# Kernel optimization log

Hardware: AMD Instinct MI355X
Metric: run time of the kernel (lower is better)

Reference implementation:

```python
import jax, jax.numpy as jnp
import numpy as np

N_A = 50000
N_B = 50000
E = 500000
D = 128


def setup_inputs() -> dict:
    key = jax.random.key(0)
    ks = jax.random.split(key, 16)
    s = 0.02
    inp = {
        "x_a": jax.random.normal(ks[0], (N_A, D), jnp.float32),
        "x_b": jax.random.normal(ks[1], (N_B, D), jnp.float32),
        # shared GraphEdgeWeight params
        "Wp": jax.random.normal(ks[2], (D, D), jnp.float32) * s,
        "bp": jnp.zeros((D,), jnp.float32),
        "Wc": jax.random.normal(ks[3], (D, D), jnp.float32) * s,
        "bc": jnp.zeros((D,), jnp.float32),
        "W1": jax.random.normal(ks[4], (D, 3 * D), jnp.float32) * s,
        "b1": jnp.zeros((D,), jnp.float32),
        "W2": jax.random.normal(ks[5], (1, D), jnp.float32) * s,
        "b2": jnp.zeros((1,), jnp.float32),
        # GraphConv params for edge type A->B
        "Wrel_ab": jax.random.normal(ks[6], (D, D), jnp.float32) * s,
        "brel_ab": jnp.zeros((D,), jnp.float32),
        "Wroot_ab": jax.random.normal(ks[7], (D, D), jnp.float32) * s,
        "broot_ab": jnp.zeros((D,), jnp.float32),
        # GraphConv params for edge type B->A
        "Wrel_ba": jax.random.normal(ks[8], (D, D), jnp.float32) * s,
        "brel_ba": jnp.zeros((D,), jnp.float32),
        "Wroot_ba": jax.random.normal(ks[9], (D, D), jnp.float32) * s,
        "broot_ba": jnp.zeros((D,), jnp.float32),
        # edge indices: row0 = src node ids, row1 = dst node ids
        "ei_ab": jax.random.randint(ks[10], (2, E), 0, N_A),
        "ei_ba": jax.random.randint(ks[11], (2, E), 0, N_B),
    }
    return inp


def _edge_type_conv(x_src, x_dst, ei, Wp, bp, Wc, bc, W1, b1, W2, b2,
                    Wrel, brel, Wroot, broot, n_dst):
    # gather endpoint features per edge  [E, D]
    par = x_src[ei[0]]
    cld = x_dst[ei[1]]
    # GraphEdgeWeight: encoders (Linear + LeakyReLU; dropout inactive in eval)
    ep = jax.nn.leaky_relu(par @ Wp.T + bp, negative_slope=0.01)
    ec = jax.nn.leaky_relu(cld @ Wc.T + bc, negative_slope=0.01)
    feat = jnp.concatenate([ep, ec, jnp.abs(par - cld)], axis=-1)  # [E, 3D]
    h = jax.nn.relu(feat @ W1.T + b1)                              # [E, D]
    w = jax.nn.sigmoid(h @ W2.T + b2)[:, 0]                        # [E]
    # GraphConv: out_i = Wrel @ sum_{j->i} w_e x_j + Wroot @ x_i (+ biases)
    msg = jax.ops.segment_sum(par * w[:, None], ei[1], num_segments=n_dst)
    return msg @ Wrel.T + brel + x_dst @ Wroot.T + broot


def reference(x_a, x_b, Wp, bp, Wc, bc, W1, b1, W2, b2,
              Wrel_ab, brel_ab, Wroot_ab, broot_ab,
              Wrel_ba, brel_ba, Wroot_ba, broot_ba,
              ei_ab, ei_ba):
    out_b = _edge_type_conv(x_a, x_b, ei_ab, Wp, bp, Wc, bc, W1, b1, W2, b2,
                            Wrel_ab, brel_ab, Wroot_ab, broot_ab, N_B)
    out_a = _edge_type_conv(x_b, x_a, ei_ba, Wp, bp, Wc, bc, W1, b1, W2, b2,
                            Wrel_ba, brel_ba, Wroot_ba, broot_ba, N_A)
    return out_a, out_b
```

## Files before the change

kernel.cpp:

```cpp
#include <hip/hip_runtime.h>
#include <hip/hip_bf16.h>

typedef unsigned short u16;
typedef __attribute__((ext_vector_type(8))) short bf16x8;
typedef __attribute__((ext_vector_type(2))) short s16x2;
typedef __attribute__((ext_vector_type(4))) float f32x4;

#define N_NODES 50000
#define EDGES 500000
#define WPT 31250
#define NWAVES 3125
#define NBLK 782

__device__ __forceinline__ u16 f2bf(float f) {
  return __builtin_bit_cast(u16, __float2bfloat16(f));
}
__device__ __forceinline__ float bf2f(u16 u) {
  return __builtin_bit_cast(float, ((unsigned)u) << 16);
}
__device__ __forceinline__ float bfe(bf16x8 v, int j) {
  return bf2f((u16)v[j]);
}

__device__ __forceinline__ void pk_atomic_bf16(u16* addr, float lo, float hi) {
#if __has_builtin(__builtin_amdgcn_global_atomic_fadd_v2bf16)
  s16x2 v;
  v[0] = (short)f2bf(lo);
  v[1] = (short)f2bf(hi);
  __builtin_amdgcn_global_atomic_fadd_v2bf16(
      (__attribute__((address_space(1))) s16x2*)addr, v);
#else
  unsigned* p = (unsigned*)addr;
  unsigned old = *p, assumed;
  do {
    assumed = old;
    float l2 = bf2f((u16)(assumed & 0xffff)) + lo;
    float h2 = bf2f((u16)(assumed >> 16)) + hi;
    unsigned nv = (unsigned)f2bf(l2) | ((unsigned)f2bf(h2) << 16);
    old = atomicCAS(p, assumed, nv);
  } while (old != assumed);
#endif
}

__global__ __launch_bounds__(256) void prep_weights(
    const float* __restrict__ Wp, const float* __restrict__ Wc,
    const float* __restrict__ W1,
    const float* __restrict__ Wrel_ab, const float* __restrict__ Wroot_ab,
    const float* __restrict__ Wrel_ba, const float* __restrict__ Wroot_ba,
    u16* __restrict__ out)
{
  int tid = blockIdx.x * 256 + threadIdx.x;
  int m = tid >> 14;
  int idx = tid & 16383;
  int r = idx >> 7;
  int c = idx & 127;
  float val;
  switch (m) {
    case 0: val = Wp[r * 128 + c]; break;
    case 1: val = Wc[r * 128 + c]; break;
    case 2: val = W1[r * 384 + c]; break;
    case 3: val = W1[r * 384 + 128 + c]; break;
    case 4: val = W1[r * 384 + 256 + c]; break;
    case 5: val = Wrel_ab[r * 128 + c]; break;
    case 6: val = Wroot_ab[r * 128 + c]; break;
    case 7: val = Wrel_ba[r * 128 + c]; break;
    default: val = Wroot_ba[r * 128 + c]; break;
  }
  out[tid] = f2bf(val);
}

__global__ __launch_bounds__(256) void cast_x(
    const float* __restrict__ xa, const float* __restrict__ xb,
    u16* __restrict__ oa, u16* __restrict__ ob)
{
  int t = blockIdx.x * 256 + threadIdx.x;
  const int HALF = (N_NODES * 128) / 8;
  const float* src;
  u16* dst;
  int idx;
  if (t < HALF) { src = xa; dst = oa; idx = t * 8; }
  else          { src = xb; dst = ob; idx = (t - HALF) * 8; }
  f32x4 a = *(const f32x4*)(src + idx);
  f32x4 b = *(const f32x4*)(src + idx + 4);
  bf16x8 o;
#pragma unroll
  for (int j = 0; j < 4; j++) {
    o[j]     = (short)f2bf(a[j]);
    o[j + 4] = (short)f2bf(b[j]);
  }
  *(bf16x8*)(dst + idx) = o;
}

__global__ __launch_bounds__(256) void encoder2(
    const u16* __restrict__ xa_bf, const u16* __restrict__ xb_bf,
    const u16* __restrict__ Wp_b, const float* __restrict__ bp,
    const u16* __restrict__ Wc_b, const float* __restrict__ bc,
    const u16* __restrict__ W1a_b, const float* __restrict__ b1,
    const u16* __restrict__ W1b_b,
    u16* __restrict__ u_a, u16* __restrict__ v_a,
    u16* __restrict__ u_b, u16* __restrict__ v_b)
{
  __shared__ u16 tile[4][2176];
  int widx = threadIdx.x >> 6;
  int w = blockIdx.x * 4 + widx;
  int type = (w >= NBLK * 4) ? 1 : 0;
  int nw = w - type * NBLK * 4;
  if (nw >= NWAVES) nw = NWAVES - 1;
  const u16* xbf = type ? xb_bf : xa_bf;
  u16* u_out = type ? u_b : u_a;
  u16* v_out = type ? v_b : v_a;
  int row0 = nw * 16;
  int lane = threadIdx.x & 63;
  int col = lane & 15;
  int quad = lane >> 4;
  u16* tl = tile[widx];

  bf16x8 af[4];
#pragma unroll
  for (int ks = 0; ks < 4; ks++)
    af[ks] = *(const bf16x8*)(xbf + (size_t)(row0 + col) * 128 + ks * 32 + quad * 8);

  f32x4 zero = {0.f, 0.f, 0.f, 0.f};

  for (int chain = 0; chain < 2; chain++) {
    const u16* Wenc = chain ? Wc_b : Wp_b;
    const float* benc = chain ? bc : bp;
    const u16* Wmix = chain ? W1b_b : W1a_b;
    const float* bmix = chain ? nullptr : b1;
    u16* outp = chain ? v_out : u_out;

    f32x4 acc[8];
#pragma unroll
    for (int nt = 0; nt < 8; nt++) acc[nt] = zero;
#pragma unroll
    for (int ks = 0; ks < 4; ks++) {
      const u16* wp = Wenc + col * 128 + ks * 32 + quad * 8;
#pragma unroll
      for (int nt = 0; nt < 8; nt++) {
        bf16x8 bf = *(const bf16x8*)(wp + nt * 2048);
        acc[nt] = __builtin_amdgcn_mfma_f32_16x16x32_bf16(af[ks], bf, acc[nt], 0, 0, 0);
      }
    }
    __syncthreads();
#pragma unroll
    for (int nt = 0; nt < 8; nt++) {
      float be = benc[nt * 16 + col];
#pragma unroll
      for (int r = 0; r < 4; r++) {
        float v = acc[nt][r] + be;
        v = v > 0.f ? v : 0.01f * v;
        tl[(quad * 4 + r) * 136 + nt * 16 + col] = f2bf(v);
      }
    }
    __syncthreads();
    bf16x8 a2[4];
#pragma unroll
    for (int ks = 0; ks < 4; ks++)
      a2[ks] = *(const bf16x8*)&tl[col * 136 + ks * 32 + quad * 8];

    f32x4 acc2[8];
#pragma unroll
    for (int nt = 0; nt < 8; nt++) acc2[nt] = zero;
#pragma unroll
    for (int ks = 0; ks < 4; ks++) {
      const u16* wp = Wmix + col * 128 + ks * 32 + quad * 8;
#pragma unroll
      for (int nt = 0; nt < 8; nt++) {
        bf16x8 bf = *(const bf16x8*)(wp + nt * 2048);
        acc2[nt] = __builtin_amdgcn_mfma_f32_16x16x32_bf16(a2[ks], bf, acc2[nt], 0, 0, 0);
      }
    }
#pragma unroll
    for (int nt = 0; nt < 8; nt++) {
      float bm = bmix ? bmix[nt * 16 + col] : 0.f;
#pragma unroll
      for (int r = 0; r < 4; r++)
        outp[(size_t)(row0 + quad * 4 + r) * 128 + nt * 16 + col] = f2bf(acc2[nt][r] + bm);
    }
  }
}

__global__ __launch_bounds__(256) void y_gemm2(
    const u16* __restrict__ xa_bf, const u16* __restrict__ xb_bf,
    const u16* __restrict__ Wrelab_b, const u16* __restrict__ Wrelba_b,
    u16* __restrict__ y_ab, u16* __restrict__ y_ba)
{
  int w = blockIdx.x * 4 + (threadIdx.x >> 6);
  int type = (w >= NBLK * 4) ? 1 : 0;
  int nw = w - type * NBLK * 4;
  if (nw >= NWAVES) return;
  const u16* xbf = type ? xb_bf : xa_bf;
  const u16* Wb = type ? Wrelba_b : Wrelab_b;
  u16* yout = type ? y_ba : y_ab;
  int row0 = nw * 16;
  int lane = threadIdx.x & 63;
  int col = lane & 15;
  int quad = lane >> 4;

  bf16x8 af[4];
#pragma unroll
  for (int ks = 0; ks < 4; ks++)
    af[ks] = *(const bf16x8*)(xbf + (size_t)(row0 + col) * 128 + ks * 32 + quad * 8);

  f32x4 zero = {0.f, 0.f, 0.f, 0.f};
  f32x4 acc[8];
#pragma unroll
  for (int nt = 0; nt < 8; nt++) acc[nt] = zero;
#pragma unroll
  for (int ks = 0; ks < 4; ks++) {
    const u16* wp = Wb + col * 128 + ks * 32 + quad * 8;
#pragma unroll
    for (int nt = 0; nt < 8; nt++) {
      bf16x8 bf = *(const bf16x8*)(wp + nt * 2048);
      acc[nt] = __builtin_amdgcn_mfma_f32_16x16x32_bf16(af[ks], bf, acc[nt], 0, 0, 0);
    }
  }
#pragma unroll
  for (int nt = 0; nt < 8; nt++)
#pragma unroll
    for (int r = 0; r < 4; r++)
      yout[(size_t)(row0 + quad * 4 + r) * 128 + nt * 16 + col] = f2bf(acc[nt][r]);
}

__global__ __launch_bounds__(256) void out_gemm2(
    const u16* __restrict__ xa_bf, const u16* __restrict__ xb_bf,
    const u16* __restrict__ msgY_a, const u16* __restrict__ msgY_b,
    const u16* __restrict__ Wrootba_b, const u16* __restrict__ Wrootab_b,
    const float* __restrict__ brel_ba, const float* __restrict__ broot_ba,
    const float* __restrict__ brel_ab, const float* __restrict__ broot_ab,
    float* __restrict__ out_a, float* __restrict__ out_b)
{
  int w = blockIdx.x * 4 + (threadIdx.x >> 6);
  int type = (w >= NBLK * 4) ? 1 : 0;
  int nw = w - type * NBLK * 4;
  if (nw >= NWAVES) return;
  const u16* xbf = type ? xb_bf : xa_bf;
  const u16* msgY = type ? msgY_b : msgY_a;
  const u16* Wb = type ? Wrootab_b : Wrootba_b;
  const float* brel = type ? brel_ab : brel_ba;
  const float* broot = type ? broot_ab : broot_ba;
  float* outp = type ? out_b : out_a;
  int row0 = nw * 16;
  int lane = threadIdx.x & 63;
  int col = lane & 15;
  int quad = lane >> 4;

  bf16x8 af[4];
#pragma unroll
  for (int ks = 0; ks < 4; ks++)
    af[ks] = *(const bf16x8*)(xbf + (size_t)(row0 + col) * 128 + ks * 32 + quad * 8);

  f32x4 zero = {0.f, 0.f, 0.f, 0.f};
  f32x4 acc[8];
#pragma unroll
  for (int nt = 0; nt < 8; nt++) acc[nt] = zero;
#pragma unroll
  for (int ks = 0; ks < 4; ks++) {
    const u16* wp = Wb + col * 128 + ks * 32 + quad * 8;
#pragma unroll
    for (int nt = 0; nt < 8; nt++) {
      bf16x8 bf = *(const bf16x8*)(wp + nt * 2048);
      acc[nt] = __builtin_amdgcn_mfma_f32_16x16x32_bf16(af[ks], bf, acc[nt], 0, 0, 0);
    }
  }
#pragma unroll
  for (int nt = 0; nt < 8; nt++) {
    int c = nt * 16 + col;
    float b = brel[c] + broot[c];
#pragma unroll
    for (int r = 0; r < 4; r++) {
      size_t row = row0 + quad * 4 + r;
      outp[row * 128 + c] = acc[nt][r] + b + bf2f(msgY[row * 128 + c]);
    }
  }
}

__global__ __launch_bounds__(256) void edge_fused(
    const u16* __restrict__ xa_bf, const u16* __restrict__ xb_bf,
    const int* __restrict__ ei_ab, const int* __restrict__ ei_ba,
    const u16* __restrict__ W1c,
    const u16* __restrict__ u_a, const u16* __restrict__ v_a,
    const u16* __restrict__ u_b, const u16* __restrict__ v_b,
    const u16* __restrict__ y_ab, const u16* __restrict__ y_ba,
    const float* __restrict__ W2, const float* __restrict__ b2p,
    u16* __restrict__ msgY_a, u16* __restrict__ msgY_b)
{
  __shared__ u16 tld[4][2176];
  int widx = threadIdx.x >> 6;
  int w = blockIdx.x * 4 + widx;
  int type = (w >= WPT) ? 1 : 0;
  int e0 = (w - type * WPT) * 16;
  const u16* xs = type ? xb_bf : xa_bf;
  const u16* xd = type ? xa_bf : xb_bf;
  const int* ei = type ? ei_ba : ei_ab;
  const u16* uT = type ? u_b : u_a;
  const u16* vT = type ? v_a : v_b;
  const u16* yT = type ? y_ba : y_ab;
  u16* msgY     = type ? msgY_a : msgY_b;

  int lane = threadIdx.x & 63;
  int col = lane & 15;
  int quad = lane >> 4;

  int em = e0 + col;
  int si = ei[em];
  int di = ei[EDGES + em];

  bf16x8 af[4];
#pragma unroll
  for (int ks = 0; ks < 4; ks++) {
    bf16x8 s8 = *(const bf16x8*)(xs + (size_t)si * 128 + ks * 32 + quad * 8);
    bf16x8 d8 = *(const bf16x8*)(xd + (size_t)di * 128 + ks * 32 + quad * 8);
#pragma unroll
    for (int j = 0; j < 8; j++)
      af[ks][j] = (short)f2bf(__builtin_fabsf(bfe(s8, j) - bfe(d8, j)));
  }

  f32x4 zero = {0.f, 0.f, 0.f, 0.f};
  f32x4 acc[8];
#pragma unroll
  for (int nt = 0; nt < 8; nt++) acc[nt] = zero;
#pragma unroll
  for (int ks = 0; ks < 4; ks++) {
    const u16* wp = W1c + col * 128 + ks * 32 + quad * 8;
#pragma unroll
    for (int nt = 0; nt < 8; nt++) {
      bf16x8 bf = *(const bf16x8*)(wp + nt * 2048);
      acc[nt] = __builtin_amdgcn_mfma_f32_16x16x32_bf16(af[ks], bf, acc[nt], 0, 0, 0);
    }
  }

  u16* tl = tld[widx];
#pragma unroll
  for (int nt = 0; nt < 8; nt++)
#pragma unroll
    for (int r = 0; r < 4; r++)
      tl[(quad * 4 + r) * 136 + nt * 16 + col] = f2bf(acc[nt][r]);
  __syncthreads();

  int e = e0 + (lane >> 2);
  int s2 = ei[e];
  int d2 = ei[EDGES + e];
  int c0 = (lane & 3) * 32;
  const u16* trow = &tl[(lane >> 2) * 136 + c0];
  const u16* urow = uT + (size_t)s2 * 128 + c0;
  const u16* vrow = vT + (size_t)d2 * 128 + c0;

  float p = 0.f;
#pragma unroll
  for (int k = 0; k < 4; k++) {
    bf16x8 tt = *(const bf16x8*)(trow + k * 8);
    bf16x8 uu = *(const bf16x8*)(urow + k * 8);
    bf16x8 vv = *(const bf16x8*)(vrow + k * 8);
    f32x4 w0 = *(const f32x4*)(W2 + c0 + k * 8);
    f32x4 w1 = *(const f32x4*)(W2 + c0 + k * 8 + 4);
#pragma unroll
    for (int j = 0; j < 4; j++) {
      float q0 = bfe(tt, j) + bfe(uu, j) + bfe(vv, j);
      if (q0 > 0.f) p += q0 * w0[j];
      float q1 = bfe(tt, j + 4) + bfe(uu, j + 4) + bfe(vv, j + 4);
      if (q1 > 0.f) p += q1 * w1[j];
    }
  }
  p += __shfl_xor(p, 1, 64);
  p += __shfl_xor(p, 2, 64);
  float wgt = 1.f / (1.f + __expf(-(p + b2p[0])));

#pragma unroll
  for (int r = 0; r < 4; r++) {
    int src_lane = (quad * 4 + r) * 4;
    float wr = __shfl(wgt, src_lane, 64);
    int sr = __shfl(s2, src_lane, 64);
    int dr = __shfl(d2, src_lane, 64);
    const u16* yrow = yT + (size_t)sr * 128;
    u16* mrow = msgY + (size_t)dr * 128;
#pragma unroll
    for (int nt = 0; nt < 4; nt++) {
      int c = nt * 32 + col * 2;
      unsigned yv = *(const unsigned*)(yrow + c);
      pk_atomic_bf16(mrow + c, wr * bf2f((u16)(yv & 0xffff)),
                               wr * bf2f((u16)(yv >> 16)));
    }
  }
}

extern "C" void kernel_launch(void* const* d_in, const int* in_sizes, int n_in,
                              void* d_out, int out_size, void* d_ws, size_t ws_size,
                              hipStream_t stream) {
  const float* x_a      = (const float*)d_in[0];
  const float* x_b      = (const float*)d_in[1];
  const float* Wp       = (const float*)d_in[2];
  const float* bp       = (const float*)d_in[3];
  const float* Wc       = (const float*)d_in[4];
  const float* bc       = (const float*)d_in[5];
  const float* W1       = (const float*)d_in[6];
  const float* b1       = (const float*)d_in[7];
  const float* W2       = (const float*)d_in[8];
  const float* b2       = (const float*)d_in[9];
  const float* Wrel_ab  = (const float*)d_in[10];
  const float* brel_ab  = (const float*)d_in[11];
  const float* Wroot_ab = (const float*)d_in[12];
  const float* broot_ab = (const float*)d_in[13];
  const float* Wrel_ba  = (const float*)d_in[14];
  const float* brel_ba  = (const float*)d_in[15];
  const float* Wroot_ba = (const float*)d_in[16];
  const float* broot_ba = (const float*)d_in[17];
  const int*   ei_ab    = (const int*)d_in[18];
  const int*   ei_ba    = (const int*)d_in[19];

  char* ws = (char*)d_ws;
  u16* Wb        = (u16*)ws;
  u16* Wp_b      = Wb + 0 * 16384;
  u16* Wc_b      = Wb + 1 * 16384;
  u16* W1a_b     = Wb + 2 * 16384;
  u16* W1b_b     = Wb + 3 * 16384;
  u16* W1c_b     = Wb + 4 * 16384;
  u16* Wrelab_b  = Wb + 5 * 16384;
  u16* Wrootab_b = Wb + 6 * 16384;
  u16* Wrelba_b  = Wb + 7 * 16384;
  u16* Wrootba_b = Wb + 8 * 16384;

  u16* xa_bf   = (u16*)(ws + 1048576);
  u16* xb_bf   = (u16*)(ws + 13848576);
  u16* u_a     = (u16*)(ws + 26648576);
  u16* v_a     = (u16*)(ws + 39448576);
  u16* u_b     = (u16*)(ws + 52248576);
  u16* v_b     = (u16*)(ws + 65048576);
  u16* y_ab    = (u16*)(ws + 77848576);
  u16* y_ba    = (u16*)(ws + 90648576);
  u16* msgY_a  = (u16*)(ws + 103448576);
  u16* msgY_b  = (u16*)(ws + 116248576);

  float* out_a = (float*)d_out;
  float* out_b = out_a + (size_t)N_NODES * 128;

  hipMemsetAsync(msgY_a, 0, (size_t)2 * N_NODES * 128 * sizeof(u16), stream);

  prep_weights<<<576, 256, 0, stream>>>(Wp, Wc, W1, Wrel_ab, Wroot_ab,
                                        Wrel_ba, Wroot_ba, Wb);
  cast_x<<<6250, 256, 0, stream>>>(x_a, x_b, xa_bf, xb_bf);

  encoder2<<<2 * NBLK, 256, 0, stream>>>(xa_bf, xb_bf, Wp_b, bp, Wc_b, bc,
                                         W1a_b, b1, W1b_b, u_a, v_a, u_b, v_b);
  y_gemm2<<<2 * NBLK, 256, 0, stream>>>(xa_bf, xb_bf, Wrelab_b, Wrelba_b, y_ab, y_ba);

  edge_fused<<<15625, 256, 0, stream>>>(xa_bf, xb_bf, ei_ab, ei_ba, W1c_b,
                                        u_a, v_a, u_b, v_b, y_ab, y_ba,
                                        W2, b2, msgY_a, msgY_b);

  out_gemm2<<<2 * NBLK, 256, 0, stream>>>(xa_bf, xb_bf, msgY_a, msgY_b,
                                          Wrootba_b, Wrootab_b,
                                          brel_ba, broot_ba, brel_ab, broot_ab,
                                          out_a, out_b);
}
```

Baseline: 772.2 us.

## Aggregate raw source features instead of pre-projected Y and fold Wrel into output GEMM

Drops the y_gemm2 pre-projection kernel. The edge kernel now scatters weighted raw source features, taken from the already-gathered xs rows held in LDS, instead of gathering a separate projected row per edge. The output GEMM then applies Wrel to the aggregated message alongside Wroot in one MFMA loop. This removes a kernel launch and a random gather of 25.6MB of y data per edge, and adds one extra GEMM over the nodes. It also removes several __syncthreads in the encoder and edge kernels, which risks LDS races because the tl buffers are per-wave.

```diff
diff --git a/kernel.cpp b/kernel.cpp
--- a/kernel.cpp
+++ b/kernel.cpp
@@ -141,7 +141,6 @@
         acc[nt] = __builtin_amdgcn_mfma_f32_16x16x32_bf16(af[ks], bf, acc[nt], 0, 0, 0);
       }
     }
-    __syncthreads();
 #pragma unroll
     for (int nt = 0; nt < 8; nt++) {
       float be = benc[nt * 16 + col];
@@ -152,7 +151,6 @@
         tl[(quad * 4 + r) * 136 + nt * 16 + col] = f2bf(v);
       }
     }
-    __syncthreads();
     bf16x8 a2[4];
 #pragma unroll
     for (int ks = 0; ks < 4; ks++)
@@ -180,51 +178,10 @@
   }
 }
 
-__global__ __launch_bounds__(256) void y_gemm2(
-    const u16* __restrict__ xa_bf, const u16* __restrict__ xb_bf,
-    const u16* __restrict__ Wrelab_b, const u16* __restrict__ Wrelba_b,
-    u16* __restrict__ y_ab, u16* __restrict__ y_ba)
-{
-  int w = blockIdx.x * 4 + (threadIdx.x >> 6);
-  int type = (w >= NBLK * 4) ? 1 : 0;
-  int nw = w - type * NBLK * 4;
-  if (nw >= NWAVES) return;
-  const u16* xbf = type ? xb_bf : xa_bf;
-  const u16* Wb = type ? Wrelba_b : Wrelab_b;
-  u16* yout = type ? y_ba : y_ab;
-  int row0 = nw * 16;
-  int lane = threadIdx.x & 63;
-  int col = lane & 15;
-  int quad = lane >> 4;
-
-  bf16x8 af[4];
-#pragma unroll
-  for (int ks = 0; ks < 4; ks++)
-    af[ks] = *(const bf16x8*)(xbf + (size_t)(row0 + col) * 128 + ks * 32 + quad * 8);
-
-  f32x4 zero = {0.f, 0.f, 0.f, 0.f};
-  f32x4 acc[8];
-#pragma unroll
-  for (int nt = 0; nt < 8; nt++) acc[nt] = zero;
-#pragma unroll
-  for (int ks = 0; ks < 4; ks++) {
-    const u16* wp = Wb + col * 128 + ks * 32 + quad * 8;
-#pragma unroll
-    for (int nt = 0; nt < 8; nt++) {
-      bf16x8 bf = *(const bf16x8*)(wp + nt * 2048);
-      acc[nt] = __builtin_amdgcn_mfma_f32_16x16x32_bf16(af[ks], bf, acc[nt], 0, 0, 0);
-    }
-  }
-#pragma unroll
-  for (int nt = 0; nt < 8; nt++)
-#pragma unroll
-    for (int r = 0; r < 4; r++)
-      yout[(size_t)(row0 + quad * 4 + r) * 128 + nt * 16 + col] = f2bf(acc[nt][r]);
-}
-
 __global__ __launch_bounds__(256) void out_gemm2(
     const u16* __restrict__ xa_bf, const u16* __restrict__ xb_bf,
-    const u16* __restrict__ msgY_a, const u16* __restrict__ msgY_b,
+    const u16* __restrict__ msgX_a, const u16* __restrict__ msgX_b,
+    const u16* __restrict__ Wrelba_b, const u16* __restrict__ Wrelab_b,
     const u16* __restrict__ Wrootba_b, const u16* __restrict__ Wrootab_b,
     const float* __restrict__ brel_ba, const float* __restrict__ broot_ba,
     const float* __restrict__ brel_ab, const float* __restrict__ broot_ab,
@@ -235,8 +192,9 @@
   int nw = w - type * NBLK * 4;
   if (nw >= NWAVES) return;
   const u16* xbf = type ? xb_bf : xa_bf;
-  const u16* msgY = type ? msgY_b : msgY_a;
-  const u16* Wb = type ? Wrootab_b : Wrootba_b;
+  const u16* msg = type ? msgX_b : msgX_a;
+  const u16* Wrel = type ? Wrelab_b : Wrelba_b;
+  const u16* Wroot = type ? Wrootab_b : Wrootba_b;
   const float* brel = type ? brel_ab : brel_ba;
   const float* broot = type ? broot_ab : broot_ba;
   float* outp = type ? out_b : out_a;
@@ -245,10 +203,12 @@
   int col = lane & 15;
   int quad = lane >> 4;
 
-  bf16x8 af[4];
-#pragma unroll
-  for (int ks = 0; ks < 4; ks++)
-    af[ks] = *(const bf16x8*)(xbf + (size_t)(row0 + col) * 128 + ks * 32 + quad * 8);
+  bf16x8 ax[4], am[4];
+#pragma unroll
+  for (int ks = 0; ks < 4; ks++) {
+    ax[ks] = *(const bf16x8*)(xbf + (size_t)(row0 + col) * 128 + ks * 32 + quad * 8);
+    am[ks] = *(const bf16x8*)(msg + (size_t)(row0 + col) * 128 + ks * 32 + quad * 8);
+  }
 
   f32x4 zero = {0.f, 0.f, 0.f, 0.f};
   f32x4 acc[8];
@@ -256,11 +216,14 @@
   for (int nt = 0; nt < 8; nt++) acc[nt] = zero;
 #pragma unroll
   for (int ks = 0; ks < 4; ks++) {
-    const u16* wp = Wb + col * 128 + ks * 32 + quad * 8;
+    const u16* wp1 = Wrel + col * 128 + ks * 32 + quad * 8;
+    const u16* wp2 = Wroot + col * 128 + ks * 32 + quad * 8;
 #pragma unroll
     for (int nt = 0; nt < 8; nt++) {
-      bf16x8 bf = *(const bf16x8*)(wp + nt * 2048);
-      acc[nt] = __builtin_amdgcn_mfma_f32_16x16x32_bf16(af[ks], bf, acc[nt], 0, 0, 0);
+      bf16x8 b1f = *(const bf16x8*)(wp1 + nt * 2048);
+      acc[nt] = __builtin_amdgcn_mfma_f32_16x16x32_bf16(am[ks], b1f, acc[nt], 0, 0, 0);
+      bf16x8 b2f = *(const bf16x8*)(wp2 + nt * 2048);
+      acc[nt] = __builtin_amdgcn_mfma_f32_16x16x32_bf16(ax[ks], b2f, acc[nt], 0, 0, 0);
     }
   }
 #pragma unroll
@@ -268,10 +231,8 @@
     int c = nt * 16 + col;
     float b = brel[c] + broot[c];
 #pragma unroll
-    for (int r = 0; r < 4; r++) {
-      size_t row = row0 + quad * 4 + r;
-      outp[row * 128 + c] = acc[nt][r] + b + bf2f(msgY[row * 128 + c]);
-    }
+    for (int r = 0; r < 4; r++)
+      outp[(size_t)(row0 + quad * 4 + r) * 128 + c] = acc[nt][r] + b;
   }
 }
 
@@ -281,9 +242,8 @@
     const u16* __restrict__ W1c,
     const u16* __restrict__ u_a, const u16* __restrict__ v_a,
     const u16* __restrict__ u_b, const u16* __restrict__ v_b,
-    const u16* __restrict__ y_ab, const u16* __restrict__ y_ba,
     const float* __restrict__ W2, const float* __restrict__ b2p,
-    u16* __restrict__ msgY_a, u16* __restrict__ msgY_b)
+    u16* __restrict__ msgX_a, u16* __restrict__ msgX_b)
 {
   __shared__ u16 tld[4][2176];
   int widx = threadIdx.x >> 6;
@@ -295,8 +255,7 @@
   const int* ei = type ? ei_ba : ei_ab;
   const u16* uT = type ? u_b : u_a;
   const u16* vT = type ? v_a : v_b;
-  const u16* yT = type ? y_ba : y_ab;
-  u16* msgY     = type ? msgY_a : msgY_b;
+  u16* msgX     = type ? msgX_a : msgX_b;
 
   int lane = threadIdx.x & 63;
   int col = lane & 15;
@@ -307,13 +266,14 @@
   int di = ei[EDGES + em];
 
   bf16x8 af[4];
+  bf16x8 df[4];
 #pragma unroll
   for (int ks = 0; ks < 4; ks++) {
-    bf16x8 s8 = *(const bf16x8*)(xs + (size_t)si * 128 + ks * 32 + quad * 8);
+    af[ks] = *(const bf16x8*)(xs + (size_t)si * 128 + ks * 32 + quad * 8);
     bf16x8 d8 = *(const bf16x8*)(xd + (size_t)di * 128 + ks * 32 + quad * 8);
 #pragma unroll
     for (int j = 0; j < 8; j++)
-      af[ks][j] = (short)f2bf(__builtin_fabsf(bfe(s8, j) - bfe(d8, j)));
+      df[ks][j] = (short)f2bf(__builtin_fabsf(bfe(af[ks], j) - bfe(d8, j)));
   }
 
   f32x4 zero = {0.f, 0.f, 0.f, 0.f};
@@ -326,7 +286,7 @@
 #pragma unroll
     for (int nt = 0; nt < 8; nt++) {
       bf16x8 bf = *(const bf16x8*)(wp + nt * 2048);
-      acc[nt] = __builtin_amdgcn_mfma_f32_16x16x32_bf16(af[ks], bf, acc[nt], 0, 0, 0);
+      acc[nt] = __builtin_amdgcn_mfma_f32_16x16x32_bf16(df[ks], bf, acc[nt], 0, 0, 0);
     }
   }
 
@@ -336,7 +296,6 @@
 #pragma unroll
     for (int r = 0; r < 4; r++)
       tl[(quad * 4 + r) * 136 + nt * 16 + col] = f2bf(acc[nt][r]);
-  __syncthreads();
 
   int e = e0 + (lane >> 2);
   int s2 = ei[e];
@@ -367,19 +326,22 @@
   float wgt = 1.f / (1.f + __expf(-(p + b2p[0])));
 
 #pragma unroll
+  for (int ks = 0; ks < 4; ks++)
+    *(bf16x8*)&tl[col * 136 + ks * 32 + quad * 8] = af[ks];
+
+#pragma unroll
   for (int r = 0; r < 4; r++) {
     int src_lane = (quad * 4 + r) * 4;
     float wr = __shfl(wgt, src_lane, 64);
-    int sr = __shfl(s2, src_lane, 64);
     int dr = __shfl(d2, src_lane, 64);
-    const u16* yrow = yT + (size_t)sr * 128;
-    u16* mrow = msgY + (size_t)dr * 128;
+    u16* mrow = msgX + (size_t)dr * 128;
+    const u16* xrow = &tl[(quad * 4 + r) * 136];
 #pragma unroll
     for (int nt = 0; nt < 4; nt++) {
       int c = nt * 32 + col * 2;
-      unsigned yv = *(const unsigned*)(yrow + c);
-      pk_atomic_bf16(mrow + c, wr * bf2f((u16)(yv & 0xffff)),
-                               wr * bf2f((u16)(yv >> 16)));
+      unsigned xv = *(const unsigned*)(xrow + c);
+      pk_atomic_bf16(mrow + c, wr * bf2f((u16)(xv & 0xffff)),
+                               wr * bf2f((u16)(xv >> 16)));
     }
   }
 }
@@ -426,15 +388,13 @@
   u16* v_a     = (u16*)(ws + 39448576);
   u16* u_b     = (u16*)(ws + 52248576);
   u16* v_b     = (u16*)(ws + 65048576);
-  u16* y_ab    = (u16*)(ws + 77848576);
-  u16* y_ba    = (u16*)(ws + 90648576);
-  u16* msgY_a  = (u16*)(ws + 103448576);
-  u16* msgY_b  = (u16*)(ws + 116248576);
+  u16* msgX_a  = (u16*)(ws + 77848576);
+  u16* msgX_b  = (u16*)(ws + 90648576);
 
   float* out_a = (float*)d_out;
   float* out_b = out_a + (size_t)N_NODES * 128;
 
-  hipMemsetAsync(msgY_a, 0, (size_t)2 * N_NODES * 128 * sizeof(u16), stream);
+  hipMemsetAsync(msgX_a, 0, (size_t)2 * N_NODES * 128 * sizeof(u16), stream);
 
   prep_weights<<<576, 256, 0, stream>>>(Wp, Wc, W1, Wrel_ab, Wroot_ab,
                                         Wrel_ba, Wroot_ba, Wb);
@@ -442,13 +402,13 @@
 
   encoder2<<<2 * NBLK, 256, 0, stream>>>(xa_bf, xb_bf, Wp_b, bp, Wc_b, bc,
                                          W1a_b, b1, W1b_b, u_a, v_a, u_b, v_b);
-  y_gemm2<<<2 * NBLK, 256, 0, stream>>>(xa_bf, xb_bf, Wrelab_b, Wrelba_b, y_ab, y_ba);
 
   edge_fused<<<15625, 256, 0, stream>>>(xa_bf, xb_bf, ei_ab, ei_ba, W1c_b,
-                                        u_a, v_a, u_b, v_b, y_ab, y_ba,
-                                        W2, b2, msgY_a, msgY_b);
-
-  out_gemm2<<<2 * NBLK, 256, 0, stream>>>(xa_bf, xb_bf, msgY_a, msgY_b,
+                                        u_a, v_a, u_b, v_b,
+                                        W2, b2, msgX_a, msgX_b);
+
+  out_gemm2<<<2 * NBLK, 256, 0, stream>>>(xa_bf, xb_bf, msgX_a, msgX_b,
+                                          Wrelba_b, Wrelab_b,
                                           Wrootba_b, Wrootab_b,
                                           brel_ba, broot_ba, brel_ab, broot_ab,
                                           out_a, out_b);
```

Measured after the change: 698.6 us. 1.11x faster.
